# Optimization experiments

Hardware: AMD Instinct MI355X
Metric: run time of the kernel (lower is better)

Reference implementation:

```python
import jax, jax.numpy as jnp
import numpy as np

B, H, W, C = 8, 224, 224, 96
WS, SHIFT, HEADS = 7, 3, 3
N = WS * WS
HEAD_DIM = C // HEADS
SCALE = HEAD_DIM ** -0.5
EPS = 1e-5


def _build_shift_mask():
    # standard Swin shifted-window attention mask, values in {0, -100}
    img = np.zeros((H, W), np.float32)
    cnt = 0
    for hs in (slice(0, -WS), slice(-WS, -SHIFT), slice(-SHIFT, None)):
        for ws_ in (slice(0, -WS), slice(-WS, -SHIFT), slice(-SHIFT, None)):
            img[hs, ws_] = cnt
            cnt += 1
    mw = img.reshape(H // WS, WS, W // WS, WS).transpose(0, 2, 1, 3).reshape(-1, N)  # (nW, N)
    am = mw[:, None, :] - mw[:, :, None]
    am = np.where(am != 0, -100.0, 0.0).astype(np.float32)  # (nW, N, N)
    return np.tile(am, (B, 1, 1))  # (B*nW, N, N)


def setup_inputs() -> dict:
    key = jax.random.key(0)
    ks = jax.random.split(key, 6)
    s = 0.02
    return {
        "x": jax.random.normal(ks[0], (B, H, W, C), jnp.float32),
        "mask": jnp.asarray(_build_shift_mask()),
        "norm1_g": jnp.ones((C,), jnp.float32),
        "norm1_b": jnp.zeros((C,), jnp.float32),
        "qkv_w": jax.random.normal(ks[1], (3 * C, C), jnp.float32) * s,
        "qkv_b": jnp.zeros((3 * C,), jnp.float32),
        "proj_w": jax.random.normal(ks[2], (C, C), jnp.float32) * s,
        "proj_b": jnp.zeros((C,), jnp.float32),
        "norm2_g": jnp.ones((C,), jnp.float32),
        "norm2_b": jnp.zeros((C,), jnp.float32),
        "fc1_w": jax.random.normal(ks[3], (4 * C, C), jnp.float32) * s,
        "fc1_b": jnp.zeros((4 * C,), jnp.float32),
        "fc2_w": jax.random.normal(ks[4], (C, 4 * C), jnp.float32) * s,
        "fc2_b": jnp.zeros((C,), jnp.float32),
    }


def _ln(x, g, b):
    mu = jnp.mean(x, axis=-1, keepdims=True)
    var = jnp.mean(jnp.square(x - mu), axis=-1, keepdims=True)
    return (x - mu) * jax.lax.rsqrt(var + EPS) * g + b


def reference(x, mask, norm1_g, norm1_b, qkv_w, qkv_b, proj_w, proj_b,
              norm2_g, norm2_b, fc1_w, fc1_b, fc2_w, fc2_b):
    b, h, w, c = x.shape
    shortcut = x.reshape(b, h * w, c)
    xn = _ln(x, norm1_g, norm1_b)
    # cyclic shift
    xs = jnp.roll(xn, (-SHIFT, -SHIFT), axis=(1, 2))
    # window partition -> (B*nW, N, C)
    xw = xs.reshape(b, h // WS, WS, w // WS, WS, c).transpose(0, 1, 3, 2, 4, 5).reshape(-1, N, c)
    # window attention
    qkv = xw @ qkv_w.T + qkv_b                                  # (B_, N, 3C)
    qkv = qkv.reshape(-1, N, 3, HEADS, HEAD_DIM).transpose(2, 0, 3, 1, 4)
    q, k, v = qkv[0] * SCALE, qkv[1], qkv[2]                    # (B_, h, N, d)
    attn = jnp.einsum('bhnd,bhmd->bhnm', q, k) + mask[:, None]  # (B_, h, N, N)
    attn = jax.nn.softmax(attn, axis=-1)
    o = jnp.einsum('bhnm,bhmd->bhnd', attn, v).transpose(0, 2, 1, 3).reshape(-1, N, c)
    o = o @ proj_w.T + proj_b
    # window reverse
    o = o.reshape(b, h // WS, w // WS, WS, WS, c).transpose(0, 1, 3, 2, 4, 5).reshape(b, h, w, c)
    o = jnp.roll(o, (SHIFT, SHIFT), axis=(1, 2)).reshape(b, h * w, c)
    x = shortcut + o
    # MLP with exact (erf) GELU, as torch nn.GELU default
    y = _ln(x, norm2_g, norm2_b)
    y = jax.nn.gelu(y @ fc1_w.T + fc1_b, approximate=False)
    return x + (y @ fc2_w.T + fc2_b)
```

## Files before the change

kernel.cpp:

```cpp
#include <hip/hip_runtime.h>

typedef __attribute__((ext_vector_type(8))) short short8;
typedef __attribute__((ext_vector_type(4))) float floatx4;

#define MFMA(a,b,c) __builtin_amdgcn_mfma_f32_16x16x32_bf16(a,b,c,0,0,0)

__device__ __forceinline__ ushort f2bf(float f){ union{float f;uint i;}x; x.f=f; return (ushort)((x.i + 0x7fffu + ((x.i>>16)&1u))>>16); }
__device__ __forceinline__ short8 lds8(const ushort* p){ return *(const short8*)p; }

__global__ void convw_kernel(const float* __restrict__ qkvw,
                             const float* __restrict__ projw,
                             const float* __restrict__ f1w,
                             const float* __restrict__ f2w,
                             ushort* __restrict__ wb)
{
  int i = blockIdx.x*256 + threadIdx.x;
  float v;
  if      (i < 27648)  v = qkvw[i];
  else if (i < 36864)  v = projw[i-27648];
  else if (i < 73728)  v = f1w[i-36864];
  else if (i < 110592) v = f2w[i-73728];
  else return;
  wb[i] = f2bf(v);
}

__global__ __launch_bounds__(256,4) void swin_block_kernel(
    const float* __restrict__ x,
    const float* __restrict__ g1, const float* __restrict__ b1v,
    const ushort* __restrict__ qkv_wb, const float* __restrict__ qkv_b,
    const ushort* __restrict__ proj_wb, const float* __restrict__ proj_b,
    const float* __restrict__ g2, const float* __restrict__ b2v,
    const ushort* __restrict__ fc1_wb, const float* __restrict__ fc1_b,
    const ushort* __restrict__ fc2_wb, const float* __restrict__ fc2_b,
    float* __restrict__ out)
{
  __shared__ __align__(16) ushort sm[19456];
  __shared__ int sid[64];
  __shared__ int spos[64];
  ushort* xn  = sm;
  ushort* Qh  = sm + 6656;
  ushort* Kh  = sm + 9216;
  ushort* Vh  = sm + 11776;
  ushort* Pb  = sm + 14080;
  float*  xrb = (float*)(sm + 6656);
  ushort* hb  = sm + 6656;

  const int tid  = threadIdx.x;
  const int w    = blockIdx.x;
  const int b    = w >> 10;
  const int wh   = (w >> 5) & 31;
  const int wwn  = w & 31;
  const int lane = tid & 63;
  const int wv   = tid >> 6;
  const int quad = lane >> 4;
  const int ln   = lane & 15;

  {
    const int n = tid >> 2, q = tid & 3;
    if (n < 49) {
      const int i = n / 7, j = n - 7*i;
      int hh = wh*7 + i + 3; if (hh >= 224) hh -= 224;
      int w2 = wwn*7 + j + 3; if (w2 >= 224) w2 -= 224;
      if (q == 0) {
        const int rr = (wh < 31) ? 0 : ((i < 4) ? 1 : 2);
        const int cr = (wwn < 31) ? 0 : ((j < 4) ? 1 : 2);
        sid[n]  = rr*3 + cr;
        spos[n] = ((b*224 + hh)*224 + w2)*96;
      }
      const float* px = x + (size_t)(((b*224 + hh)*224 + w2)*96) + q*24;
      float v[24]; float s = 0.f, s2 = 0.f;
      const float4* p4 = (const float4*)px;
      #pragma unroll
      for (int t = 0; t < 6; ++t) { float4 u = p4[t];
        v[t*4+0]=u.x; v[t*4+1]=u.y; v[t*4+2]=u.z; v[t*4+3]=u.w; }
      #pragma unroll
      for (int c = 0; c < 24; ++c) { s += v[c]; s2 += v[c]*v[c]; }
      s  += __shfl_xor(s, 1);  s  += __shfl_xor(s, 2);
      s2 += __shfl_xor(s2, 1); s2 += __shfl_xor(s2, 2);
      const float mu = s * (1.f/96.f);
      const float rs = rsqrtf(s2*(1.f/96.f) - mu*mu + 1e-5f);
      ushort* row = xn + n*104 + q*24;
      #pragma unroll
      for (int c = 0; c < 24; ++c)
        row[c] = f2bf((v[c]-mu)*rs*g1[q*24+c] + b1v[q*24+c]);
    }
    for (int idx = tid; idx < 15*104; idx += 256) xn[49*104 + idx] = 0;
  }
  __syncthreads();

  short8 a_[12];
  #pragma unroll
  for (int rt = 0; rt < 4; ++rt)
    #pragma unroll
    for (int k = 0; k < 3; ++k)
      a_[rt*3+k] = lds8(xn + (rt*16 + ln)*104 + k*32 + quad*8);

  int idrv[4], idcv[4];
  #pragma unroll
  for (int reg = 0; reg < 4; ++reg) {
    const int r = wv*16 + quad*4 + reg;
    idrv[reg] = (r < 49) ? sid[r] : -1;
  }
  #pragma unroll
  for (int nt = 0; nt < 4; ++nt) {
    const int c = nt*16 + ln;
    idcv[nt] = (c < 49) ? sid[c] : -2;
  }

  ushort* ob = xn;
  for (int h = 0; h < 3; ++h) {
    {
      const int sec  = wv >> 1;
      const int sub  = wv & 1;
      const int colw = sec*96 + h*32 + sub*16 + ln;
      const ushort* wr = qkv_wb + colw*96 + quad*8;
      short8 b0 = lds8(wr), b1 = lds8(wr+32), b2 = lds8(wr+64);
      const int colv = 192 + h*32 + (wv>>1)*16 + ln;
      const ushort* wr2 = qkv_wb + colv*96 + quad*8;
      short8 c0 = lds8(wr2), c1 = lds8(wr2+32), c2 = lds8(wr2+64);
      const float biasA = qkv_b[colw];
      const float biasV = qkv_b[colv];
      const int d  = sub*16 + ln;
      const int dv = (wv>>1)*16 + ln;
      #pragma unroll
      for (int rt = 0; rt < 4; ++rt) {
        floatx4 acc = {0.f,0.f,0.f,0.f};
        acc = MFMA(a_[rt*3+0], b0, acc);
        acc = MFMA(a_[rt*3+1], b1, acc);
        acc = MFMA(a_[rt*3+2], b2, acc);
        #pragma unroll
        for (int reg = 0; reg < 4; ++reg) {
          const int r = rt*16 + quad*4 + reg;
          const float val = acc[reg] + biasA;
          if (sec == 0) Qh[r*40 + d] = f2bf(val * 0.17677669529663689f);
          else          Kh[r*40 + d] = f2bf(val);
        }
      }
      const int rt0 = (wv & 1)*2;
      #pragma unroll
      for (int j = 0; j < 2; ++j) {
        floatx4 acc = {0.f,0.f,0.f,0.f};
        acc = MFMA(a_[(rt0+j)*3+0], c0, acc);
        acc = MFMA(a_[(rt0+j)*3+1], c1, acc);
        acc = MFMA(a_[(rt0+j)*3+2], c2, acc);
        #pragma unroll
        for (int reg = 0; reg < 4; ++reg) {
          const int r = (rt0+j)*16 + quad*4 + reg;
          Vh[dv*72 + r] = f2bf(acc[reg] + biasV);
        }
      }
    }
    __syncthreads();

    {
      short8 aq = lds8(Qh + (wv*16 + ln)*40 + quad*8);
      floatx4 sc[4];
      #pragma unroll
      for (int nt = 0; nt < 4; ++nt) {
        short8 kb = lds8(Kh + (nt*16 + ln)*40 + quad*8);
        floatx4 z = {0.f,0.f,0.f,0.f};
        sc[nt] = MFMA(aq, kb, z);
      }
      #pragma unroll
      for (int reg = 0; reg < 4; ++reg) {
        float t[4]; float mx = -1e30f;
        #pragma unroll
        for (int nt = 0; nt < 4; ++nt) {
          float tv = -1e30f;
          if (idrv[reg] >= 0 && idcv[nt] >= 0)
            tv = sc[nt][reg] + ((idrv[reg] == idcv[nt]) ? 0.f : -100.f);
          t[nt] = tv; mx = fmaxf(mx, tv);
        }
        mx = fmaxf(mx, __shfl_xor(mx, 1));
        mx = fmaxf(mx, __shfl_xor(mx, 2));
        mx = fmaxf(mx, __shfl_xor(mx, 4));
        mx = fmaxf(mx, __shfl_xor(mx, 8));
        float e[4], sum = 0.f;
        #pragma unroll
        for (int nt = 0; nt < 4; ++nt) {
          e[nt] = (t[nt] > -1e29f) ? __expf(t[nt] - mx) : 0.f;
          sum += e[nt];
        }
        sum += __shfl_xor(sum, 1);
        sum += __shfl_xor(sum, 2);
        sum += __shfl_xor(sum, 4);
        sum += __shfl_xor(sum, 8);
        const float inv = (sum > 0.f) ? 1.f/sum : 0.f;
        #pragma unroll
        for (int nt = 0; nt < 4; ++nt)
          Pb[(wv*16 + quad*4 + reg)*72 + nt*16 + ln] = f2bf(e[nt]*inv);
      }
    }
    __syncthreads();

    {
      short8 p0 = lds8(Pb + (wv*16 + ln)*72 + quad*8);
      short8 p1 = lds8(Pb + (wv*16 + ln)*72 + 32 + quad*8);
      #pragma unroll
      for (int ntd = 0; ntd < 2; ++ntd) {
        floatx4 accO = {0.f,0.f,0.f,0.f};
        accO = MFMA(p0, lds8(Vh + (ntd*16+ln)*72 + quad*8),      accO);
        accO = MFMA(p1, lds8(Vh + (ntd*16+ln)*72 + 32 + quad*8), accO);
        #pragma unroll
        for (int reg = 0; reg < 4; ++reg)
          ob[(wv*16 + quad*4 + reg)*104 + h*32 + ntd*16 + ln] = f2bf(accO[reg]);
      }
    }
    __syncthreads();
  }

  {
    short8 o_[12];
    #pragma unroll
    for (int rt = 0; rt < 4; ++rt)
      #pragma unroll
      for (int k = 0; k < 3; ++k)
        o_[rt*3+k] = lds8(ob + (rt*16 + ln)*104 + k*32 + quad*8);

    const int colA = wv*16 + ln;
    const ushort* wr = proj_wb + colA*96 + quad*8;
    short8 b0 = lds8(wr), b1 = lds8(wr+32), b2 = lds8(wr+64);
    const int colB = (4 + (wv>>1))*16 + ln;
    const ushort* wr2 = proj_wb + colB*96 + quad*8;
    short8 c0 = lds8(wr2), c1 = lds8(wr2+32), c2 = lds8(wr2+64);
    const float biasA = proj_b[colA], biasB = proj_b[colB];

    #pragma unroll
    for (int rt = 0; rt < 4; ++rt) {
      floatx4 acc = {0.f,0.f,0.f,0.f};
      acc = MFMA(o_[rt*3+0], b0, acc);
      acc = MFMA(o_[rt*3+1], b1, acc);
      acc = MFMA(o_[rt*3+2], b2, acc);
      #pragma unroll
      for (int reg = 0; reg < 4; ++reg) {
        const int r = rt*16 + quad*4 + reg;
        if (r < 49) {
          const int pos = spos[r] + colA;
          const float val = x[pos] + acc[reg] + biasA;
          xrb[r*96 + colA] = val;
          out[pos] = val;
        }
      }
    }
    const int rt0 = (wv & 1)*2;
    #pragma unroll
    for (int j = 0; j < 2; ++j) {
      floatx4 acc = {0.f,0.f,0.f,0.f};
      acc = MFMA(o_[(rt0+j)*3+0], c0, acc);
      acc = MFMA(o_[(rt0+j)*3+1], c1, acc);
      acc = MFMA(o_[(rt0+j)*3+2], c2, acc);
      #pragma unroll
      for (int reg = 0; reg < 4; ++reg) {
        const int r = (rt0+j)*16 + quad*4 + reg;
        if (r < 49) {
          const int pos = spos[r] + colB;
          const float val = x[pos] + acc[reg] + biasB;
          xrb[r*96 + colB] = val;
          out[pos] = val;
        }
      }
    }
    for (int idx = tid; idx < 15*96; idx += 256) xrb[49*96 + idx] = 0.f;
  }
  __syncthreads();

  {
    const int n = tid >> 2, q = tid & 3;
    const float4* p4 = (const float4*)(xrb + n*96 + q*24);
    float v[24]; float s = 0.f, s2 = 0.f;
    #pragma unroll
    for (int t = 0; t < 6; ++t) { float4 u = p4[t];
      v[t*4+0]=u.x; v[t*4+1]=u.y; v[t*4+2]=u.z; v[t*4+3]=u.w; }
    #pragma unroll
    for (int c = 0; c < 24; ++c) { s += v[c]; s2 += v[c]*v[c]; }
    s  += __shfl_xor(s, 1);  s  += __shfl_xor(s, 2);
    s2 += __shfl_xor(s2, 1); s2 += __shfl_xor(s2, 2);
    const float mu = s * (1.f/96.f);
    const float rs = rsqrtf(s2*(1.f/96.f) - mu*mu + 1e-5f);
    ushort* row = xn + n*104 + q*24;
    #pragma unroll
    for (int c = 0; c < 24; ++c)
      row[c] = f2bf((v[c]-mu)*rs*g2[q*24+c] + b2v[q*24+c]);
  }
  __syncthreads();

  floatx4 Cacc[3][2];
  #pragma unroll
  for (int t = 0; t < 3; ++t)
    #pragma unroll
    for (int j = 0; j < 2; ++j)
      Cacc[t][j] = (floatx4){0.f,0.f,0.f,0.f};
  const int p  = wv >> 1;
  const int cg = (wv & 1)*3;

  for (int ch = 0; ch < 2; ++ch) {
    {
      short8 m_[12];
      #pragma unroll
      for (int rt = 0; rt < 4; ++rt)
        #pragma unroll
        for (int k = 0; k < 3; ++k)
          m_[rt*3+k] = lds8(xn + (rt*16 + ln)*104 + k*32 + quad*8);
      #pragma unroll
      for (int t = 0; t < 3; ++t) {
        const int ntl  = wv*3 + t;
        const int colh = ntl*16 + ln;
        const int gcol = ch*192 + colh;
        const ushort* wr1 = fc1_wb + gcol*96 + quad*8;
        short8 b0 = lds8(wr1), b1 = lds8(wr1+32), b2 = lds8(wr1+64);
        const float bias = fc1_b[gcol];
        #pragma unroll
        for (int rt = 0; rt < 4; ++rt) {
          floatx4 acc = {0.f,0.f,0.f,0.f};
          acc = MFMA(m_[rt*3+0], b0, acc);
          acc = MFMA(m_[rt*3+1], b1, acc);
          acc = MFMA(m_[rt*3+2], b2, acc);
          #pragma unroll
          for (int reg = 0; reg < 4; ++reg) {
            const float vv = acc[reg] + bias;
            hb[(rt*16 + quad*4 + reg)*200 + colh] =
                f2bf(0.5f*vv*(1.f + erff(vv*0.70710678118654752f)));
          }
        }
      }
    }
    __syncthreads();
    {
      short8 h_[12];
      #pragma unroll
      for (int j = 0; j < 2; ++j)
        #pragma unroll
        for (int k = 0; k < 6; ++k)
          h_[j*6+k] = lds8(hb + ((2*p+j)*16 + ln)*200 + k*32 + quad*8);
      #pragma unroll
      for (int t = 0; t < 3; ++t) {
        const int outc = (cg + t)*16 + ln;
        const ushort* wr2 = fc2_wb + outc*384 + ch*192 + quad*8;
        short8 w0 = lds8(wr2),     w1 = lds8(wr2+32),  w2 = lds8(wr2+64),
               w3 = lds8(wr2+96),  w4 = lds8(wr2+128), w5 = lds8(wr2+160);
        #pragma unroll
        for (int j = 0; j < 2; ++j) {
          floatx4 acc = Cacc[t][j];
          acc = MFMA(h_[j*6+0], w0, acc);
          acc = MFMA(h_[j*6+1], w1, acc);
          acc = MFMA(h_[j*6+2], w2, acc);
          acc = MFMA(h_[j*6+3], w3, acc);
          acc = MFMA(h_[j*6+4], w4, acc);
          acc = MFMA(h_[j*6+5], w5, acc);
          Cacc[t][j] = acc;
        }
      }
    }
    __syncthreads();
  }

  #pragma unroll
  for (int t = 0; t < 3; ++t) {
    const int outc = (cg + t)*16 + ln;
    const float bias = fc2_b[outc];
    #pragma unroll
    for (int j = 0; j < 2; ++j) {
      #pragma unroll
      for (int reg = 0; reg < 4; ++reg) {
        const int r = (2*p + j)*16 + quad*4 + reg;
        if (r < 49) {
          const int pos = spos[r] + outc;
          out[pos] += Cacc[t][j][reg] + bias;
        }
      }
    }
  }
}

extern "C" void kernel_launch(void* const* d_in, const int* in_sizes, int n_in,
                              void* d_out, int out_size, void* d_ws, size_t ws_size,
                              hipStream_t stream) {
  int ix=-1, iq=-1, ip=-1, if1=-1, if2=-1, largest=0;
  for (int i = 0; i < n_in; ++i) {
    const int s = in_sizes[i];
    if (s == 38535168 && ix < 0) ix = i;
    else if (s == 27648 && iq < 0) iq = i;
    else if (s == 9216 && ip < 0) ip = i;
    else if (s == 36864) { if (if1 < 0) if1 = i; else if (if2 < 0) if2 = i; }
    if (in_sizes[i] >= in_sizes[largest]) largest = i;
  }
  if (ix < 0) ix = largest;
  if (iq < 0) iq = 4;
  if (ip < 0) ip = 6;
  if (if1 < 0) if1 = 10;
  if (if2 < 0) if2 = 12;

  const float* x    = (const float*)d_in[ix];
  const float* n1g  = (const float*)d_in[2];
  const float* n1b  = (const float*)d_in[3];
  const float* qkvw = (const float*)d_in[iq];
  const float* qkvb = (const float*)d_in[5];
  const float* pw   = (const float*)d_in[ip];
  const float* pb   = (const float*)d_in[7];
  const float* n2g  = (const float*)d_in[8];
  const float* n2b  = (const float*)d_in[9];
  const float* f1w  = (const float*)d_in[if1];
  const float* f1b  = (const float*)d_in[11];
  const float* f2w  = (const float*)d_in[if2];
  const float* f2b  = (const float*)d_in[13];
  float* outp = (float*)d_out;
  ushort* wb = (ushort*)d_ws;

  convw_kernel<<<432, 256, 0, stream>>>(qkvw, pw, f1w, f2w, wb);
  swin_block_kernel<<<8192, 256, 0, stream>>>(
      x, n1g, n1b, wb, qkvb, wb + 27648, pb,
      n2g, n2b, wb + 36864, f1b, wb + 73728, f2b, outp);
}
```

Baseline: 961.1 us.

## Make each wavefront own 16 rows end-to-end, removing block barriers in proj/MLP

Each wavefront now handles one 16-row tile from the attention output through the projection, LayerNorm2, fc1+GELU and fc2. GELU activations go through a private per-wave staging buffer, so the block-wide __syncthreads between phases are dropped. The residual is kept in LDS and the final output is written once, which removes the global out write-then-read-modify-write. Shared memory grows and the launch bounds drop to 3 blocks per CU. Every wave now reads all weight columns itself, so each weight row is fetched four times per block instead of once.

```diff
diff --git a/kernel.cpp b/kernel.cpp
--- a/kernel.cpp
+++ b/kernel.cpp
@@ -24,7 +24,7 @@
   wb[i] = f2bf(v);
 }
 
-__global__ __launch_bounds__(256,4) void swin_block_kernel(
+__global__ __launch_bounds__(256,3) void swin_block_kernel(
     const float* __restrict__ x,
     const float* __restrict__ g1, const float* __restrict__ b1v,
     const ushort* __restrict__ qkv_wb, const float* __restrict__ qkv_b,
@@ -34,7 +34,7 @@
     const ushort* __restrict__ fc2_wb, const float* __restrict__ fc2_b,
     float* __restrict__ out)
 {
-  __shared__ __align__(16) ushort sm[19456];
+  __shared__ __align__(16) ushort sm[23112];
   __shared__ int sid[64];
   __shared__ int spos[64];
   ushort* xn  = sm;
@@ -43,7 +43,7 @@
   ushort* Vh  = sm + 11776;
   ushort* Pb  = sm + 14080;
   float*  xrb = (float*)(sm + 6656);
-  ushort* hb  = sm + 6656;
+  ushort* stg = sm + 16456;
 
   const int tid  = threadIdx.x;
   const int w    = blockIdx.x;
@@ -56,7 +56,8 @@
   const int ln   = lane & 15;
 
   {
-    const int n = tid >> 2, q = tid & 3;
+    const int n = wv*16 + (lane >> 2);
+    const int q = lane & 3;
     if (n < 49) {
       const int i = n / 7, j = n - 7*i;
       int hh = wh*7 + i + 3; if (hh >= 224) hh -= 224;
@@ -84,7 +85,8 @@
       for (int c = 0; c < 24; ++c)
         row[c] = f2bf((v[c]-mu)*rs*g1[q*24+c] + b1v[q*24+c]);
     }
-    for (int idx = tid; idx < 15*104; idx += 256) xn[49*104 + idx] = 0;
+    if (wv == 3)
+      for (int idx = lane; idx < 15*104; idx += 64) xn[49*104 + idx] = 0;
   }
   __syncthreads();
 
@@ -191,8 +193,6 @@
           Pb[(wv*16 + quad*4 + reg)*72 + nt*16 + ln] = f2bf(e[nt]*inv);
       }
     }
-    __syncthreads();
-
     {
       short8 p0 = lds8(Pb + (wv*16 + ln)*72 + quad*8);
       short8 p1 = lds8(Pb + (wv*16 + ln)*72 + 32 + quad*8);
@@ -210,67 +210,39 @@
   }
 
   {
-    short8 o_[12];
-    #pragma unroll
-    for (int rt = 0; rt < 4; ++rt)
-      #pragma unroll
-      for (int k = 0; k < 3; ++k)
-        o_[rt*3+k] = lds8(ob + (rt*16 + ln)*104 + k*32 + quad*8);
-
-    const int colA = wv*16 + ln;
-    const ushort* wr = proj_wb + colA*96 + quad*8;
-    short8 b0 = lds8(wr), b1 = lds8(wr+32), b2 = lds8(wr+64);
-    const int colB = (4 + (wv>>1))*16 + ln;
-    const ushort* wr2 = proj_wb + colB*96 + quad*8;
-    short8 c0 = lds8(wr2), c1 = lds8(wr2+32), c2 = lds8(wr2+64);
-    const float biasA = proj_b[colA], biasB = proj_b[colB];
-
-    #pragma unroll
-    for (int rt = 0; rt < 4; ++rt) {
+    const ushort* arow = ob + (wv*16 + ln)*104 + quad*8;
+    short8 o0 = lds8(arow), o1 = lds8(arow+32), o2 = lds8(arow+64);
+    #pragma unroll
+    for (int nt = 0; nt < 6; ++nt) {
+      const int col = nt*16 + ln;
+      const ushort* wr = proj_wb + col*96 + quad*8;
       floatx4 acc = {0.f,0.f,0.f,0.f};
-      acc = MFMA(o_[rt*3+0], b0, acc);
-      acc = MFMA(o_[rt*3+1], b1, acc);
-      acc = MFMA(o_[rt*3+2], b2, acc);
+      acc = MFMA(o0, lds8(wr),    acc);
+      acc = MFMA(o1, lds8(wr+32), acc);
+      acc = MFMA(o2, lds8(wr+64), acc);
+      const float bias = proj_b[col];
       #pragma unroll
       for (int reg = 0; reg < 4; ++reg) {
-        const int r = rt*16 + quad*4 + reg;
-        if (r < 49) {
-          const int pos = spos[r] + colA;
-          const float val = x[pos] + acc[reg] + biasA;
-          xrb[r*96 + colA] = val;
-          out[pos] = val;
-        }
-      }
-    }
-    const int rt0 = (wv & 1)*2;
-    #pragma unroll
-    for (int j = 0; j < 2; ++j) {
-      floatx4 acc = {0.f,0.f,0.f,0.f};
-      acc = MFMA(o_[(rt0+j)*3+0], c0, acc);
-      acc = MFMA(o_[(rt0+j)*3+1], c1, acc);
-      acc = MFMA(o_[(rt0+j)*3+2], c2, acc);
-      #pragma unroll
-      for (int reg = 0; reg < 4; ++reg) {
-        const int r = (rt0+j)*16 + quad*4 + reg;
-        if (r < 49) {
-          const int pos = spos[r] + colB;
-          const float val = x[pos] + acc[reg] + biasB;
-          xrb[r*96 + colB] = val;
-          out[pos] = val;
-        }
-      }
-    }
-    for (int idx = tid; idx < 15*96; idx += 256) xrb[49*96 + idx] = 0.f;
-  }
-  __syncthreads();
+        const int r = wv*16 + quad*4 + reg;
+        if (r < 49)
+          xrb[r*100 + col] = x[spos[r] + col] + acc[reg] + bias;
+      }
+    }
+  }
 
   {
-    const int n = tid >> 2, q = tid & 3;
-    const float4* p4 = (const float4*)(xrb + n*96 + q*24);
-    float v[24]; float s = 0.f, s2 = 0.f;
-    #pragma unroll
-    for (int t = 0; t < 6; ++t) { float4 u = p4[t];
-      v[t*4+0]=u.x; v[t*4+1]=u.y; v[t*4+2]=u.z; v[t*4+3]=u.w; }
+    const int n = wv*16 + (lane >> 2);
+    const int q = lane & 3;
+    float v[24];
+    #pragma unroll
+    for (int c = 0; c < 24; ++c) v[c] = 0.f;
+    if (n < 49) {
+      const float4* p4 = (const float4*)(xrb + n*100 + q*24);
+      #pragma unroll
+      for (int t = 0; t < 6; ++t) { float4 u = p4[t];
+        v[t*4+0]=u.x; v[t*4+1]=u.y; v[t*4+2]=u.z; v[t*4+3]=u.w; }
+    }
+    float s = 0.f, s2 = 0.f;
     #pragma unroll
     for (int c = 0; c < 24; ++c) { s += v[c]; s2 += v[c]*v[c]; }
     s  += __shfl_xor(s, 1);  s  += __shfl_xor(s, 2);
@@ -282,91 +254,56 @@
     for (int c = 0; c < 24; ++c)
       row[c] = f2bf((v[c]-mu)*rs*g2[q*24+c] + b2v[q*24+c]);
   }
-  __syncthreads();
-
-  floatx4 Cacc[3][2];
-  #pragma unroll
-  for (int t = 0; t < 3; ++t)
-    #pragma unroll
-    for (int j = 0; j < 2; ++j)
-      Cacc[t][j] = (floatx4){0.f,0.f,0.f,0.f};
-  const int p  = wv >> 1;
-  const int cg = (wv & 1)*3;
-
-  for (int ch = 0; ch < 2; ++ch) {
-    {
-      short8 m_[12];
-      #pragma unroll
-      for (int rt = 0; rt < 4; ++rt)
-        #pragma unroll
-        for (int k = 0; k < 3; ++k)
-          m_[rt*3+k] = lds8(xn + (rt*16 + ln)*104 + k*32 + quad*8);
-      #pragma unroll
-      for (int t = 0; t < 3; ++t) {
-        const int ntl  = wv*3 + t;
-        const int colh = ntl*16 + ln;
-        const int gcol = ch*192 + colh;
+
+  {
+    ushort* stgw = stg + wv*1664;
+    const ushort* arow = xn + (wv*16 + ln)*104 + quad*8;
+    short8 m0 = lds8(arow), m1 = lds8(arow+32), m2 = lds8(arow+64);
+    floatx4 Cacc[6];
+    #pragma unroll
+    for (int ot = 0; ot < 6; ++ot) Cacc[ot] = (floatx4){0.f,0.f,0.f,0.f};
+
+    for (int ch = 0; ch < 4; ++ch) {
+      #pragma unroll
+      for (int t = 0; t < 6; ++t) {
+        const int gcol = ch*96 + t*16 + ln;
         const ushort* wr1 = fc1_wb + gcol*96 + quad*8;
-        short8 b0 = lds8(wr1), b1 = lds8(wr1+32), b2 = lds8(wr1+64);
+        floatx4 acc = {0.f,0.f,0.f,0.f};
+        acc = MFMA(m0, lds8(wr1),    acc);
+        acc = MFMA(m1, lds8(wr1+32), acc);
+        acc = MFMA(m2, lds8(wr1+64), acc);
         const float bias = fc1_b[gcol];
         #pragma unroll
-        for (int rt = 0; rt < 4; ++rt) {
-          floatx4 acc = {0.f,0.f,0.f,0.f};
-          acc = MFMA(m_[rt*3+0], b0, acc);
-          acc = MFMA(m_[rt*3+1], b1, acc);
-          acc = MFMA(m_[rt*3+2], b2, acc);
-          #pragma unroll
-          for (int reg = 0; reg < 4; ++reg) {
-            const float vv = acc[reg] + bias;
-            hb[(rt*16 + quad*4 + reg)*200 + colh] =
-                f2bf(0.5f*vv*(1.f + erff(vv*0.70710678118654752f)));
-          }
-        }
-      }
-    }
-    __syncthreads();
-    {
-      short8 h_[12];
-      #pragma unroll
-      for (int j = 0; j < 2; ++j)
-        #pragma unroll
-        for (int k = 0; k < 6; ++k)
-          h_[j*6+k] = lds8(hb + ((2*p+j)*16 + ln)*200 + k*32 + quad*8);
-      #pragma unroll
-      for (int t = 0; t < 3; ++t) {
-        const int outc = (cg + t)*16 + ln;
-        const ushort* wr2 = fc2_wb + outc*384 + ch*192 + quad*8;
-        short8 w0 = lds8(wr2),     w1 = lds8(wr2+32),  w2 = lds8(wr2+64),
-               w3 = lds8(wr2+96),  w4 = lds8(wr2+128), w5 = lds8(wr2+160);
-        #pragma unroll
-        for (int j = 0; j < 2; ++j) {
-          floatx4 acc = Cacc[t][j];
-          acc = MFMA(h_[j*6+0], w0, acc);
-          acc = MFMA(h_[j*6+1], w1, acc);
-          acc = MFMA(h_[j*6+2], w2, acc);
-          acc = MFMA(h_[j*6+3], w3, acc);
-          acc = MFMA(h_[j*6+4], w4, acc);
-          acc = MFMA(h_[j*6+5], w5, acc);
-          Cacc[t][j] = acc;
-        }
-      }
-    }
-    __syncthreads();
-  }
-
-  #pragma unroll
-  for (int t = 0; t < 3; ++t) {
-    const int outc = (cg + t)*16 + ln;
-    const float bias = fc2_b[outc];
-    #pragma unroll
-    for (int j = 0; j < 2; ++j) {
+        for (int reg = 0; reg < 4; ++reg) {
+          const float vv = acc[reg] + bias;
+          stgw[(quad*4 + reg)*104 + t*16 + ln] =
+              f2bf(0.5f*vv*(1.f + erff(vv*0.70710678118654752f)));
+        }
+      }
+      short8 s0 = lds8(stgw + ln*104 + quad*8);
+      short8 s1 = lds8(stgw + ln*104 + 32 + quad*8);
+      short8 s2 = lds8(stgw + ln*104 + 64 + quad*8);
+      #pragma unroll
+      for (int ot = 0; ot < 6; ++ot) {
+        const int outc = ot*16 + ln;
+        const ushort* wr2 = fc2_wb + outc*384 + ch*96 + quad*8;
+        floatx4 acc = Cacc[ot];
+        acc = MFMA(s0, lds8(wr2),    acc);
+        acc = MFMA(s1, lds8(wr2+32), acc);
+        acc = MFMA(s2, lds8(wr2+64), acc);
+        Cacc[ot] = acc;
+      }
+    }
+
+    #pragma unroll
+    for (int ot = 0; ot < 6; ++ot) {
+      const int outc = ot*16 + ln;
+      const float bias = fc2_b[outc];
       #pragma unroll
       for (int reg = 0; reg < 4; ++reg) {
-        const int r = (2*p + j)*16 + quad*4 + reg;
-        if (r < 49) {
-          const int pos = spos[r] + outc;
-          out[pos] += Cacc[t][j][reg] + bias;
-        }
+        const int r = wv*16 + quad*4 + reg;
+        if (r < 49)
+          out[spos[r] + outc] = xrb[r*100 + outc] + Cacc[ot][reg] + bias;
       }
     }
   }
```

Result: slower. 1.104 ms (+14.8%).
